# Performance work log

Measured on AMD Instinct MI355X. Metric: run time of the kernel, lower is better.

## Reference

```python
import jax, jax.numpy as jnp
import numpy as np

B, C, H, W = 8, 512, 64, 64
NH = 8
HD = C // NH
EPS = 1e-5


def _bn(x, w, b):
    # training-mode BatchNorm2d: batch stats over (B,H,W), biased variance
    mean = jnp.mean(x, axis=(0, 2, 3), keepdims=True)
    var = jnp.var(x, axis=(0, 2, 3), keepdims=True)
    return (x - mean) * jax.lax.rsqrt(var + EPS) * w[None, :, None, None] + b[None, :, None, None]


def setup_inputs() -> dict:
    key = jax.random.key(0)
    ks = jax.random.split(key, 8)
    s = 1.0 / np.sqrt(C)
    return {
        "x": jax.random.normal(ks[0], (B, C, H, W), dtype=jnp.float32),
        "q_w": jax.random.normal(ks[1], (C, C), dtype=jnp.float32) * s,
        "k_w": jax.random.normal(ks[2], (C, C), dtype=jnp.float32) * s,
        "v_w": jax.random.normal(ks[3], (C, C), dtype=jnp.float32) * s,
        "temperature": jnp.ones((NH, 1, 1), dtype=jnp.float32),
        "gamma": jnp.full((1,), 0.5, dtype=jnp.float32),
        "bn_in_w": jnp.ones((C,), dtype=jnp.float32),
        "bn_in_b": jnp.zeros((C,), dtype=jnp.float32),
        "bn_out_w": jnp.ones((C,), dtype=jnp.float32),
        "bn_out_b": jnp.zeros((C,), dtype=jnp.float32),
    }


def reference(x, q_w, k_w, v_w, temperature, gamma, bn_in_w, bn_in_b, bn_out_w, bn_out_b):
    xn = _bn(x, bn_in_w, bn_in_b)
    # 1x1 convs == channel-mixing linear maps
    q = jnp.einsum('oc,bchw->bohw', q_w, xn)
    k = jnp.einsum('oc,bchw->bohw', k_w, xn)
    v = jnp.einsum('oc,bchw->bohw', v_w, xn)
    # 2D FFT over spatial dims -> complex64
    q_f = jnp.fft.fft2(q)
    k_f = jnp.fft.fft2(k)
    v_f = jnp.fft.fft2(v)
    # b (h c) H W -> b h c (H W)
    qh = q_f.reshape(B, NH, HD, H * W)
    kh = k_f.reshape(B, NH, HD, H * W)
    vh = v_f.reshape(B, NH, HD, H * W)
    # complex channel-attention scores [B, NH, HD, HD]
    attn = jnp.einsum('bhcn,bhdn->bhcd', qh, kh) * temperature[None]
    # complex softmax: softmax over real and imag parts independently
    attn = jax.lax.complex(jax.nn.softmax(attn.real, axis=-1),
                           jax.nn.softmax(attn.imag, axis=-1))
    out_f = jnp.einsum('bhcd,bhdn->bhcn', attn, vh)
    out_f = out_f.reshape(B, C, H, W)
    out = jnp.fft.ifft2(out_f).real
    out = x + gamma * out
    return _bn(out, bn_out_w, bn_out_b)
```

## Files before the change

kernel.cpp:

```cpp
#include <hip/hip_runtime.h>
#include <math.h>

#define NB 8
#define NC 512
#define NHW 4096
#define NNH 8
#define BN_EPS 1e-5f

typedef __attribute__((ext_vector_type(8))) short bf16x8;
typedef __attribute__((ext_vector_type(4))) float f32x4;
typedef __attribute__((ext_vector_type(4))) short s16x4;
typedef __attribute__((ext_vector_type(2))) short s16x2;
typedef unsigned short ushort_t;

__device__ __forceinline__ ushort_t bf16r(float f) {
    unsigned u = __float_as_uint(f);
    return (ushort_t)((u + 0x7fffu + ((u >> 16) & 1u)) >> 16);
}
__device__ __forceinline__ float bf16f(ushort_t h) {
    return __uint_as_float(((unsigned)h) << 16);
}
__device__ __forceinline__ void split3(float v, ushort_t& h1, ushort_t& h2, ushort_t& h3) {
    h1 = bf16r(v); float r = v - bf16f(h1);
    h2 = bf16r(r); r -= bf16f(h2);
    h3 = bf16r(r);
}
__device__ __forceinline__ void split2(float v, ushort_t& h1, ushort_t& h2) {
    h1 = bf16r(v); float r = v - bf16f(h1);
    h2 = bf16r(r);
}

__global__ __launch_bounds__(256) void fa_bn_stats(const float* __restrict__ src,
                                                   const float* __restrict__ w,
                                                   const float* __restrict__ bb,
                                                   float* __restrict__ ss) {
    int c = blockIdx.x;
    int t = threadIdx.x;
    float s = 0.f, sq = 0.f;
    for (int b = 0; b < NB; ++b) {
        const float4* p = (const float4*)(src + ((size_t)(b * NC + c)) * NHW);
        for (int i = t; i < NHW / 4; i += 256) {
            float4 v = p[i];
            s += v.x + v.y + v.z + v.w;
            sq += v.x * v.x + v.y * v.y + v.z * v.z + v.w * v.w;
        }
    }
#pragma unroll
    for (int off = 32; off; off >>= 1) {
        s += __shfl_down(s, off, 64);
        sq += __shfl_down(sq, off, 64);
    }
    __shared__ float ls[4], lq[4];
    int wid = t >> 6, lane = t & 63;
    if (lane == 0) { ls[wid] = s; lq[wid] = sq; }
    __syncthreads();
    if (t == 0) {
        float S = ls[0] + ls[1] + ls[2] + ls[3];
        float Q = lq[0] + lq[1] + lq[2] + lq[3];
        float n = (float)(NB * NHW);
        float mean = S / n;
        float var = Q / n - mean * mean;
        float r = rsqrtf(var + BN_EPS);
        float sc = r * w[c];
        ss[c] = sc;
        ss[NC + c] = bb[c] - mean * sc;
    }
}

__global__ __launch_bounds__(256) void fa_bn2_fin(const float* __restrict__ st,
                                                  const float* __restrict__ w,
                                                  const float* __restrict__ bb,
                                                  float* __restrict__ ss) {
    int c = blockIdx.x * 256 + threadIdx.x;
    float S = st[c], Q = st[512 + c];
    float n = (float)(NB * NHW);
    float mean = S / n;
    float var = Q / n - mean * mean;
    float r = rsqrtf(var + BN_EPS);
    float sc = r * w[c];
    ss[c] = sc;
    ss[NC + c] = bb[c] - mean * sc;
}

__global__ __launch_bounds__(256) void fa_split(const float* __restrict__ x,
                                                const float* __restrict__ ss,
                                                short* __restrict__ X0, short* __restrict__ X1,
                                                short* __restrict__ R0, short* __restrict__ R1) {
    int b = blockIdx.x >> 9, c = blockIdx.x & 511;
    float sc = ss[c], sh = ss[NC + c];
    size_t o = ((size_t)(b * NC + c)) * NHW;
    const float4* src = (const float4*)(x + o);
    __shared__ float xf[NHW];
    int t = threadIdx.x;
#pragma unroll
    for (int k = 0; k < 4; ++k) {
        int i4 = t + k * 256;
        float4 v = src[i4];
        s16x4 p0, p1;
#pragma unroll
        for (int j = 0; j < 4; ++j) {
            float xn = fmaf(((const float*)&v)[j], sc, sh);
            xf[4 * i4 + j] = xn;
            ushort_t h0, h1;
            split2(xn, h0, h1);
            p0[j] = (short)h0; p1[j] = (short)h1;
        }
        *(s16x4*)&X0[o + 4 * i4] = p0;
        *(s16x4*)&X1[o + 4 * i4] = p1;
    }
    __syncthreads();
#pragma unroll
    for (int k = 0; k < 4; ++k) {
        int i4 = t + k * 256;
        s16x4 p0, p1;
#pragma unroll
        for (int j = 0; j < 4; ++j) {
            int u = 4 * i4 + j;
            int rev = (((64 - (u >> 6)) & 63) << 6) | ((64 - (u & 63)) & 63);
            float xn = xf[rev];
            ushort_t h0, h1;
            split2(xn, h0, h1);
            p0[j] = (short)h0; p1[j] = (short)h1;
        }
        *(s16x4*)&R0[o + 4 * i4] = p0;
        *(s16x4*)&R1[o + 4 * i4] = p1;
    }
}

__global__ __launch_bounds__(256) void fa_wsplit_qk(const float* __restrict__ qw,
                                                    const float* __restrict__ kw,
                                                    short* __restrict__ Q0, short* __restrict__ Q1,
                                                    short* __restrict__ Q2,
                                                    short* __restrict__ K0p, short* __restrict__ K1p,
                                                    short* __restrict__ K2p) {
    int r = blockIdx.x, m = blockIdx.y;
    const float* src = m ? kw : qw;
    short* P0 = m ? K0p : Q0;
    short* P1 = m ? K1p : Q1;
    short* P2 = m ? K2p : Q2;
    int t = threadIdx.x;
    float2 v = *(const float2*)&src[(size_t)r * NC + 2 * t];
    s16x2 p0, p1, p2;
    ushort_t a, bq, cq;
    split3(v.x, a, bq, cq); p0[0] = (short)a; p1[0] = (short)bq; p2[0] = (short)cq;
    split3(v.y, a, bq, cq); p0[1] = (short)a; p1[1] = (short)bq; p2[1] = (short)cq;
    size_t o = (size_t)r * NC + 2 * t;
    *(s16x2*)&P0[o] = p0;
    *(s16x2*)&P1[o] = p1;
    *(s16x2*)&P2[o] = p2;
}

__global__ __launch_bounds__(256) void fa_wsplit_vt(const float* __restrict__ vw,
                                                    short* __restrict__ V0, short* __restrict__ V1) {
    __shared__ float tile[64][65];
    int hd0 = blockIdx.x * 64, cc0 = blockIdx.y * 64;
    int t = threadIdx.x;
#pragma unroll
    for (int k = 0; k < 16; ++k) {
        int idx = t + k * 256;
        int r = idx >> 6, c = idx & 63;
        tile[r][c] = vw[(size_t)(hd0 + r) * NC + cc0 + c];
    }
    __syncthreads();
#pragma unroll
    for (int k = 0; k < 16; ++k) {
        int idx = t + k * 256;
        int r = idx >> 6, c = idx & 63;
        float v = tile[c][r];
        ushort_t a, bq;
        split2(v, a, bq);
        size_t o = (size_t)(cc0 + r) * NC + hd0 + c;
        V0[o] = (short)a; V1[o] = (short)bq;
    }
}

#define GSTR 40
__global__ __launch_bounds__(256, 2) void fa_gram5(
    const short* __restrict__ X0, const short* __restrict__ X1,
    const short* __restrict__ R0, const short* __restrict__ R1,
    float* __restrict__ Gs) {
    static const char PI[10] = {0, 0, 0, 0, 1, 1, 1, 2, 2, 3};
    static const char PJ[10] = {0, 1, 2, 3, 1, 2, 3, 2, 3, 3};
    __shared__ __align__(16) short A0[128 * GSTR], A1[128 * GSTR];
    __shared__ __align__(16) short B0[128 * GSTR], B1[128 * GSTR];
    const int bid = blockIdx.x;
    const int flat = (bid & 7) * 40 + (bid >> 3);
    const int p = flat % 10;
    const int rem = flat / 10;
    const int kq = rem & 3;
    const int b = rem >> 2;
    const int c1t = PI[p] * 128, c2t = PJ[p] * 128;
    const int t = threadIdx.x, lane = t & 63, wv = t >> 6;
    const int row = t >> 1, half = (t & 1) * 16;
    const int lo = row * GSTR + half;
    const size_t kb0 = (size_t)kq * 1024;
    const short* pA0 = X0 + ((size_t)(b * NC + c1t + row)) * NHW + half + kb0;
    const short* pA1 = X1 + ((size_t)(b * NC + c1t + row)) * NHW + half + kb0;
    const short* pB0 = R0 + ((size_t)(b * NC + c2t + row)) * NHW + half + kb0;
    const short* pB1 = R1 + ((size_t)(b * NC + c2t + row)) * NHW + half + kb0;
    const int wrow = (wv >> 1) * 64, wcol = (wv & 1) * 64;
    const int frow = lane & 15, koff = (lane >> 4) * 8;

    f32x4 acc[4][4];
#pragma unroll
    for (int i = 0; i < 4; ++i)
#pragma unroll
        for (int j = 0; j < 4; ++j) {
            f32x4 z = {0.f, 0.f, 0.f, 0.f};
            acc[i][j] = z;
        }

    bf16x8 rA0a = *(const bf16x8*)&pA0[0], rA0b = *(const bf16x8*)&pA0[8];
    bf16x8 rA1a = *(const bf16x8*)&pA1[0], rA1b = *(const bf16x8*)&pA1[8];
    bf16x8 rB0a = *(const bf16x8*)&pB0[0], rB0b = *(const bf16x8*)&pB0[8];
    bf16x8 rB1a = *(const bf16x8*)&pB1[0], rB1b = *(const bf16x8*)&pB1[8];

#pragma unroll 1
    for (int s = 0; s < 32; ++s) {
        __syncthreads();
        *(bf16x8*)&A0[lo] = rA0a; *(bf16x8*)&A0[lo + 8] = rA0b;
        *(bf16x8*)&A1[lo] = rA1a; *(bf16x8*)&A1[lo + 8] = rA1b;
        *(bf16x8*)&B0[lo] = rB0a; *(bf16x8*)&B0[lo + 8] = rB0b;
        *(bf16x8*)&B1[lo] = rB1a; *(bf16x8*)&B1[lo + 8] = rB1b;
        __syncthreads();
        if (s < 31) {
            pA0 += 32; pA1 += 32; pB0 += 32; pB1 += 32;
            rA0a = *(const bf16x8*)&pA0[0]; rA0b = *(const bf16x8*)&pA0[8];
            rA1a = *(const bf16x8*)&pA1[0]; rA1b = *(const bf16x8*)&pA1[8];
            rB0a = *(const bf16x8*)&pB0[0]; rB0b = *(const bf16x8*)&pB0[8];
            rB1a = *(const bf16x8*)&pB1[0]; rB1b = *(const bf16x8*)&pB1[8];
        }
        bf16x8 a0[4], a1[4];
#pragma unroll
        for (int fr = 0; fr < 4; ++fr) {
            int o = (wrow + fr * 16 + frow) * GSTR + koff;
            a0[fr] = *(const bf16x8*)&A0[o];
            a1[fr] = *(const bf16x8*)&A1[o];
        }
        {
            bf16x8 bv[4];
#pragma unroll
            for (int fc = 0; fc < 4; ++fc)
                bv[fc] = *(const bf16x8*)&B0[(wcol + fc * 16 + frow) * GSTR + koff];
#pragma unroll
            for (int fr = 0; fr < 4; ++fr)
#pragma unroll
                for (int fc = 0; fc < 4; ++fc) {
                    acc[fr][fc] = __builtin_amdgcn_mfma_f32_16x16x32_bf16(a0[fr], bv[fc], acc[fr][fc], 0, 0, 0);
                    acc[fr][fc] = __builtin_amdgcn_mfma_f32_16x16x32_bf16(a1[fr], bv[fc], acc[fr][fc], 0, 0, 0);
                }
        }
        {
            bf16x8 bv[4];
#pragma unroll
            for (int fc = 0; fc < 4; ++fc)
                bv[fc] = *(const bf16x8*)&B1[(wcol + fc * 16 + frow) * GSTR + koff];
#pragma unroll
            for (int fr = 0; fr < 4; ++fr)
#pragma unroll
                for (int fc = 0; fc < 4; ++fc)
                    acc[fr][fc] = __builtin_amdgcn_mfma_f32_16x16x32_bf16(a0[fr], bv[fc], acc[fr][fc], 0, 0, 0);
        }
    }
    float* Gsl = Gs + (size_t)kq * 2097152;
    const bool diag = (c1t == c2t);
#pragma unroll
    for (int fr = 0; fr < 4; ++fr)
#pragma unroll
        for (int fc = 0; fc < 4; ++fc)
#pragma unroll
            for (int j = 0; j < 4; ++j) {
                int r1 = c1t + wrow + fr * 16 + (lane >> 4) * 4 + j;
                int r2 = c2t + wcol + fc * 16 + frow;
                float v = acc[fr][fc][j];
                Gsl[((size_t)(b * NC) + r1) * NC + r2] = v;
                if (!diag) Gsl[((size_t)(b * NC) + r2) * NC + r1] = v;
            }
}

__global__ __launch_bounds__(256) void fa_gsplit(const float* __restrict__ Gs,
                                                 short* __restrict__ Gp0, short* __restrict__ Gp1,
                                                 short* __restrict__ Gp2) {
    size_t i = ((size_t)blockIdx.x * 256 + threadIdx.x) * 8;
    f32x4 s0 = *(const f32x4*)&Gs[i];
    f32x4 s1 = *(const f32x4*)&Gs[i + 4];
#pragma unroll
    for (int k = 1; k < 4; ++k) {
        s0 += *(const f32x4*)&Gs[(size_t)k * 2097152 + i];
        s1 += *(const f32x4*)&Gs[(size_t)k * 2097152 + i + 4];
    }
    bf16x8 p0, p1, p2;
#pragma unroll
    for (int j = 0; j < 4; ++j) {
        ushort_t a, bq, cq;
        split3(s0[j], a, bq, cq);
        p0[j] = (short)a; p1[j] = (short)bq; p2[j] = (short)cq;
        split3(s1[j], a, bq, cq);
        p0[4 + j] = (short)a; p1[4 + j] = (short)bq; p2[4 + j] = (short)cq;
    }
    *(bf16x8*)&Gp0[i] = p0;
    *(bf16x8*)&Gp1[i] = p1;
    *(bf16x8*)&Gp2[i] = p2;
}

__global__ __launch_bounds__(256, 2) void fa_attn2(
    const short* __restrict__ Gp0, const short* __restrict__ Gp1, const short* __restrict__ Gp2,
    const short* __restrict__ Q0, const short* __restrict__ Q1, const short* __restrict__ Q2,
    const short* __restrict__ Kp0, const short* __restrict__ Kp1, const short* __restrict__ Kp2,
    float* __restrict__ P) {
    __shared__ __align__(16) short Aq0[64 * GSTR], Aq1[64 * GSTR], Aq2[64 * GSTR];
    __shared__ __align__(16) short Bg0[64 * GSTR], Bg1[64 * GSTR], Bg2[64 * GSTR];
    __shared__ __align__(16) float Tf[64 * 68];
    const int chunk = blockIdx.x, h = blockIdx.y, b = blockIdx.z;
    const int t = threadIdx.x, lane = t & 63, wv = t >> 6;
    const int srow = t >> 2, sq = (t & 3) * 8;
    const int frow = lane & 15, koff = (lane >> 4) * 8;
    const int wrow = (wv >> 1) * 32, wcol = (wv & 1) * 32;
    const int slo = srow * GSTR + sq;
    const size_t qbase = ((size_t)(h * 64 + srow)) * NC + sq;
    const size_t gbase = ((size_t)(b * NC + chunk * 64 + srow)) * NC + sq;

    f32x4 acc[2][2];
#pragma unroll
    for (int i = 0; i < 2; ++i)
#pragma unroll
        for (int j = 0; j < 2; ++j) {
            f32x4 z = {0.f, 0.f, 0.f, 0.f};
            acc[i][j] = z;
        }
    for (int K0 = 0; K0 < NC; K0 += 32) {
        __syncthreads();
        *(bf16x8*)&Aq0[slo] = *(const bf16x8*)&Q0[qbase + K0];
        *(bf16x8*)&Aq1[slo] = *(const bf16x8*)&Q1[qbase + K0];
        *(bf16x8*)&Aq2[slo] = *(const bf16x8*)&Q2[qbase + K0];
        *(bf16x8*)&Bg0[slo] = *(const bf16x8*)&Gp0[gbase + K0];
        *(bf16x8*)&Bg1[slo] = *(const bf16x8*)&Gp1[gbase + K0];
        *(bf16x8*)&Bg2[slo] = *(const bf16x8*)&Gp2[gbase + K0];
        __syncthreads();
        bf16x8 a0[2], a1[2], a2[2];
#pragma unroll
        for (int fr = 0; fr < 2; ++fr) {
            int o = (wrow + fr * 16 + frow) * GSTR + koff;
            a0[fr] = *(const bf16x8*)&Aq0[o];
            a1[fr] = *(const bf16x8*)&Aq1[o];
            a2[fr] = *(const bf16x8*)&Aq2[o];
        }
#pragma unroll
        for (int fc = 0; fc < 2; ++fc) {
            int o = (wcol + fc * 16 + frow) * GSTR + koff;
            bf16x8 b0 = *(const bf16x8*)&Bg0[o];
            bf16x8 b1 = *(const bf16x8*)&Bg1[o];
            bf16x8 b2 = *(const bf16x8*)&Bg2[o];
#pragma unroll
            for (int fr = 0; fr < 2; ++fr) {
                acc[fr][fc] = __builtin_amdgcn_mfma_f32_16x16x32_bf16(a0[fr], b0, acc[fr][fc], 0, 0, 0);
                acc[fr][fc] = __builtin_amdgcn_mfma_f32_16x16x32_bf16(a1[fr], b0, acc[fr][fc], 0, 0, 0);
                acc[fr][fc] = __builtin_amdgcn_mfma_f32_16x16x32_bf16(a2[fr], b0, acc[fr][fc], 0, 0, 0);
                acc[fr][fc] = __builtin_amdgcn_mfma_f32_16x16x32_bf16(a0[fr], b1, acc[fr][fc], 0, 0, 0);
                acc[fr][fc] = __builtin_amdgcn_mfma_f32_16x16x32_bf16(a1[fr], b1, acc[fr][fc], 0, 0, 0);
                acc[fr][fc] = __builtin_amdgcn_mfma_f32_16x16x32_bf16(a0[fr], b2, acc[fr][fc], 0, 0, 0);
            }
        }
    }
#pragma unroll
    for (int fr = 0; fr < 2; ++fr)
#pragma unroll
        for (int fc = 0; fc < 2; ++fc)
#pragma unroll
            for (int j = 0; j < 4; ++j)
                Tf[(wrow + fr * 16 + (lane >> 4) * 4 + j) * 68 + wcol + fc * 16 + frow] = acc[fr][fc][j];

    f32x4 acc2[4];
#pragma unroll
    for (int j = 0; j < 4; ++j) {
        f32x4 z = {0.f, 0.f, 0.f, 0.f};
        acc2[j] = z;
    }
    for (int kw = 0; kw < 2; ++kw) {
        __syncthreads();
        size_t kb = ((size_t)(h * 64 + srow)) * NC + chunk * 64 + kw * 32 + sq;
        *(bf16x8*)&Bg0[slo] = *(const bf16x8*)&Kp0[kb];
        *(bf16x8*)&Bg1[slo] = *(const bf16x8*)&Kp1[kb];
        *(bf16x8*)&Bg2[slo] = *(const bf16x8*)&Kp2[kb];
        __syncthreads();
        f32x4 u0 = *(const f32x4*)&Tf[(wv * 16 + frow) * 68 + kw * 32 + koff];
        f32x4 u1 = *(const f32x4*)&Tf[(wv * 16 + frow) * 68 + kw * 32 + koff + 4];
        bf16x8 t0, t1, t2;
#pragma unroll
        for (int j = 0; j < 4; ++j) {
            ushort_t a, bq, cq;
            split3(u0[j], a, bq, cq);
            t0[j] = (short)a; t1[j] = (short)bq; t2[j] = (short)cq;
            split3(u1[j], a, bq, cq);
            t0[4 + j] = (short)a; t1[4 + j] = (short)bq; t2[4 + j] = (short)cq;
        }
#pragma unroll
        for (int fc = 0; fc < 4; ++fc) {
            int o = (fc * 16 + frow) * GSTR + koff;
            bf16x8 b0 = *(const bf16x8*)&Bg0[o];
            bf16x8 b1 = *(const bf16x8*)&Bg1[o];
            bf16x8 b2 = *(const bf16x8*)&Bg2[o];
            acc2[fc] = __builtin_amdgcn_mfma_f32_16x16x32_bf16(t0, b0, acc2[fc], 0, 0, 0);
            acc2[fc] = __builtin_amdgcn_mfma_f32_16x16x32_bf16(t1, b0, acc2[fc], 0, 0, 0);
            acc2[fc] = __builtin_amdgcn_mfma_f32_16x16x32_bf16(t2, b0, acc2[fc], 0, 0, 0);
            acc2[fc] = __builtin_amdgcn_mfma_f32_16x16x32_bf16(t0, b1, acc2[fc], 0, 0, 0);
            acc2[fc] = __builtin_amdgcn_mfma_f32_16x16x32_bf16(t1, b1, acc2[fc], 0, 0, 0);
            acc2[fc] = __builtin_amdgcn_mfma_f32_16x16x32_bf16(t0, b2, acc2[fc], 0, 0, 0);
        }
    }
    size_t base = (((size_t)(b * NNH + h)) * 8 + chunk) * 4096;
#pragma unroll
    for (int fc = 0; fc < 4; ++fc)
#pragma unroll
        for (int j = 0; j < 4; ++j) {
            int row = wv * 16 + (lane >> 4) * 4 + j;
            int col = fc * 16 + frow;
            P[base + row * 64 + col] = acc2[fc][j];
        }
}

__global__ __launch_bounds__(256, 1) void fa_fin2(const float* __restrict__ P,
                                                  const float* __restrict__ temp,
                                                  const short* __restrict__ V0,
                                                  const short* __restrict__ V1,
                                                  short* __restrict__ M0) {
    __shared__ float Asm[64 * 68];
    const int h = blockIdx.x, b = blockIdx.y;
    const int t = threadIdx.x, lane = t & 63, wv = t >> 6;
    const float tv = temp[h] * (float)NHW;
    const float* pb = P + ((size_t)(b * NNH + h)) * 8 * 4096;
    for (int i = t; i < 4096; i += 256) {
        float s = 0.f;
#pragma unroll
        for (int ch = 0; ch < 8; ++ch) s += pb[ch * 4096 + i];
        Asm[(i >> 6) * 68 + (i & 63)] = s * tv;
    }
    __syncthreads();
    {
        int row = t >> 2, base = row * 68 + (t & 3) * 16;
        float m = -1e30f;
#pragma unroll
        for (int j = 0; j < 16; ++j) m = fmaxf(m, Asm[base + j]);
        m = fmaxf(m, __shfl_xor(m, 1, 64));
        m = fmaxf(m, __shfl_xor(m, 2, 64));
        float s = 0.f;
#pragma unroll
        for (int j = 0; j < 16; ++j) {
            float e = __expf(Asm[base + j] - m);
            Asm[base + j] = e;
            s += e;
        }
        s += __shfl_xor(s, 1, 64);
        s += __shfl_xor(s, 2, 64);
        float inv = 1.0f / s;
#pragma unroll
        for (int j = 0; j < 16; ++j) Asm[base + j] *= inv;
    }
    __syncthreads();
    const int frow = lane & 15, koff = (lane >> 4) * 8;
    bf16x8 a0[4][2], a1[4][2];
#pragma unroll
    for (int fr = 0; fr < 4; ++fr)
#pragma unroll
        for (int kw = 0; kw < 2; ++kw) {
            f32x4 u0 = *(const f32x4*)&Asm[(fr * 16 + frow) * 68 + kw * 32 + koff];
            f32x4 u1 = *(const f32x4*)&Asm[(fr * 16 + frow) * 68 + kw * 32 + koff + 4];
#pragma unroll
            for (int j = 0; j < 4; ++j) {
                ushort_t a, bq;
                split2(u0[j], a, bq);
                a0[fr][kw][j] = (short)a; a1[fr][kw][j] = (short)bq;
                split2(u1[j], a, bq);
                a0[fr][kw][4 + j] = (short)a; a1[fr][kw][4 + j] = (short)bq;
            }
        }
    for (int half = 0; half < 2; ++half) {
        int cb = wv * 128 + half * 64;
        f32x4 acc[4][4];
#pragma unroll
        for (int i = 0; i < 4; ++i)
#pragma unroll
            for (int j = 0; j < 4; ++j) {
                f32x4 z = {0.f, 0.f, 0.f, 0.f};
                acc[i][j] = z;
            }
#pragma unroll
        for (int fc = 0; fc < 4; ++fc)
#pragma unroll
            for (int kw = 0; kw < 2; ++kw) {
                size_t vb = (size_t)(cb + fc * 16 + frow) * NC + h * 64 + kw * 32 + koff;
                bf16x8 b0 = *(const bf16x8*)&V0[vb];
                bf16x8 b1 = *(const bf16x8*)&V1[vb];
#pragma unroll
                for (int fr = 0; fr < 4; ++fr) {
                    acc[fr][fc] = __builtin_amdgcn_mfma_f32_16x16x32_bf16(a0[fr][kw], b0, acc[fr][fc], 0, 0, 0);
                    acc[fr][fc] = __builtin_amdgcn_mfma_f32_16x16x32_bf16(a0[fr][kw], b1, acc[fr][fc], 0, 0, 0);
                    acc[fr][fc] = __builtin_amdgcn_mfma_f32_16x16x32_bf16(a1[fr][kw], b0, acc[fr][fc], 0, 0, 0);
                }
            }
#pragma unroll
        for (int fr = 0; fr < 4; ++fr)
#pragma unroll
            for (int fc = 0; fc < 4; ++fc)
#pragma unroll
                for (int j = 0; j < 4; ++j) {
                    int row = fr * 16 + (lane >> 4) * 4 + j;
                    int cc = cb + fc * 16 + frow;
                    size_t o = ((size_t)(b * NC + h * 64 + row)) * NC + cc;
                    M0[o] = (short)bf16r(acc[fr][fc][j]);
                }
    }
}

#define OSTR2 72
__global__ __launch_bounds__(256, 4) void fa_out4(const float* __restrict__ x,
                                                  const short* __restrict__ M0,
                                                  const short* __restrict__ X0,
                                                  const float* __restrict__ gamma,
                                                  float* __restrict__ y,
                                                  float* __restrict__ st) {
    __shared__ __align__(16) short Am[128 * OSTR2];
    __shared__ __align__(16) short Bx[128 * OSTR2];
    const int s0 = blockIdx.x * 128, c0 = blockIdx.y * 128, b = blockIdx.z;
    const int t = threadIdx.x, lane = t & 63, wv = t >> 6;
    const int arow = t >> 1, ah = (t & 1) * 32;
    const int cc0 = (t & 31) * 2, sb = (t >> 5) * 16;
    const int frow = lane & 15, koff = (lane >> 4) * 8;
    const int wrow = (wv >> 1) * 64, wcol = (wv & 1) * 64;
    const size_t mbase = ((size_t)(b * NC + c0 + arow)) * NC + ah;
    const size_t xbase = ((size_t)(b * NC + cc0)) * NHW + s0 + sb;

    f32x4 acc[4][4];
#pragma unroll
    for (int i = 0; i < 4; ++i)
#pragma unroll
        for (int j = 0; j < 4; ++j) {
            f32x4 z = {0.f, 0.f, 0.f, 0.f};
            acc[i][j] = z;
        }

    bf16x8 mA[4], xA[4];
#pragma unroll
    for (int q = 0; q < 4; ++q) mA[q] = *(const bf16x8*)&M0[mbase + 8 * q];
    xA[0] = *(const bf16x8*)&X0[xbase];
    xA[1] = *(const bf16x8*)&X0[xbase + 8];
    xA[2] = *(const bf16x8*)&X0[xbase + NHW];
    xA[3] = *(const bf16x8*)&X0[xbase + NHW + 8];

#pragma unroll 1
    for (int K0 = 0; K0 < NC; K0 += 64) {
        __syncthreads();
#pragma unroll
        for (int q = 0; q < 4; ++q)
            *(bf16x8*)&Am[arow * OSTR2 + ah + 8 * q] = mA[q];
#pragma unroll
        for (int si = 0; si < 8; ++si) {
            s16x2 pv; pv[0] = xA[0][si]; pv[1] = xA[2][si];
            *(s16x2*)&Bx[(sb + si) * OSTR2 + cc0] = pv;
            s16x2 qv; qv[0] = xA[1][si]; qv[1] = xA[3][si];
            *(s16x2*)&Bx[(sb + 8 + si) * OSTR2 + cc0] = qv;
        }
        __syncthreads();
        if (K0 < NC - 64) {
            const size_t mb = mbase + K0 + 64;
            const size_t xb = xbase + (size_t)(K0 + 64) * NHW;
#pragma unroll
            for (int q = 0; q < 4; ++q) mA[q] = *(const bf16x8*)&M0[mb + 8 * q];
            xA[0] = *(const bf16x8*)&X0[xb];
            xA[1] = *(const bf16x8*)&X0[xb + 8];
            xA[2] = *(const bf16x8*)&X0[xb + NHW];
            xA[3] = *(const bf16x8*)&X0[xb + NHW + 8];
        }
#pragma unroll
        for (int kw = 0; kw < 2; ++kw) {
            int ko = kw * 32 + koff;
            bf16x8 a0[4], b0[4];
#pragma unroll
            for (int fr = 0; fr < 4; ++fr)
                a0[fr] = *(const bf16x8*)&Am[(wrow + fr * 16 + frow) * OSTR2 + ko];
#pragma unroll
            for (int fc = 0; fc < 4; ++fc)
                b0[fc] = *(const bf16x8*)&Bx[(wcol + fc * 16 + frow) * OSTR2 + ko];
#pragma unroll
            for (int fr = 0; fr < 4; ++fr)
#pragma unroll
                for (int fc = 0; fc < 4; ++fc)
                    acc[fr][fc] = __builtin_amdgcn_mfma_f32_16x16x32_bf16(a0[fr], b0[fc], acc[fr][fc], 0, 0, 0);
        }
    }
    float g = gamma[0];
    float sY[16], sQ[16];
#pragma unroll
    for (int i = 0; i < 16; ++i) { sY[i] = 0.f; sQ[i] = 0.f; }
#pragma unroll
    for (int fr = 0; fr < 4; ++fr)
#pragma unroll
        for (int fc = 0; fc < 4; ++fc)
#pragma unroll
            for (int j = 0; j < 4; ++j) {
                int c = c0 + wrow + fr * 16 + (lane >> 4) * 4 + j;
                int s = s0 + wcol + fc * 16 + frow;
                size_t idx = ((size_t)(b * NC + c)) * NHW + s;
                float v = x[idx] + g * acc[fr][fc][j];
                y[idx] = v;
                sY[fr * 4 + j] += v;
                sQ[fr * 4 + j] += v * v;
            }
#pragma unroll
    for (int i = 0; i < 16; ++i) {
#pragma unroll
        for (int off = 1; off < 16; off <<= 1) {
            sY[i] += __shfl_xor(sY[i], off, 64);
            sQ[i] += __shfl_xor(sQ[i], off, 64);
        }
    }
    if (frow == 0) {
#pragma unroll
        for (int i = 0; i < 16; ++i) {
            int c = c0 + wrow + (i >> 2) * 16 + (lane >> 4) * 4 + (i & 3);
            atomicAdd(&st[c], sY[i]);
            atomicAdd(&st[512 + c], sQ[i]);
        }
    }
}

__global__ __launch_bounds__(256) void fa_bn_apply(float* __restrict__ y,
                                                   const float* __restrict__ ss) {
    const float* scale = ss;
    const float* shift = ss + NC;
    const long long total4 = (long long)NB * NC * NHW / 4;
    for (long long i4 = (long long)blockIdx.x * blockDim.x + threadIdx.x; i4 < total4;
         i4 += (long long)gridDim.x * blockDim.x) {
        int c = (int)((i4 >> 10) & (NC - 1));
        float4 v = ((const float4*)y)[i4];
        float sc = scale[c], sh = shift[c];
        v.x = v.x * sc + sh;
        v.y = v.y * sc + sh;
        v.z = v.z * sc + sh;
        v.w = v.w * sc + sh;
        ((float4*)y)[i4] = v;
    }
}

__device__ __forceinline__ int swz(int row, int kk) {
    return ((kk >> 2) ^ (row >> 2)) * 4 + (kk & 3);
}
__device__ __forceinline__ void mm_tile(const float* __restrict__ As,
                                        const float* __restrict__ Bs,
                                        int tr, int tc, float (&acc)[4][4]) {
#pragma unroll
    for (int k4 = 0; k4 < 16; ++k4) {
        float4 a[4], bv[4];
#pragma unroll
        for (int i = 0; i < 4; ++i)
            a[i] = *(const float4*)&As[(tr * 4 + i) * 64 + (((k4 ^ tr) & 15) << 2)];
#pragma unroll
        for (int j = 0; j < 4; ++j)
            bv[j] = *(const float4*)&Bs[(tc * 4 + j) * 64 + (((k4 ^ tc) & 15) << 2)];
#pragma unroll
        for (int i = 0; i < 4; ++i)
#pragma unroll
            for (int j = 0; j < 4; ++j)
                acc[i][j] += a[i].x * bv[j].x + a[i].y * bv[j].y +
                             a[i].z * bv[j].z + a[i].w * bv[j].w;
    }
}
__global__ __launch_bounds__(256, 2) void fa_gram_mfma(const float* __restrict__ x,
                                                       const float* __restrict__ ss,
                                                       float* __restrict__ G) {
    __shared__ __align__(16) short As0[128 * GSTR], As1[128 * GSTR], As2[128 * GSTR];
    __shared__ __align__(16) short Bs0[128 * GSTR], Bs1[128 * GSTR], Bs2[128 * GSTR];
    const int c2t = blockIdx.x * 128;
    const int c1t = blockIdx.y * 128;
    const int b = blockIdx.z >> 2;
    const int kq = blockIdx.z & 3;
    const int t = threadIdx.x;
    const int lane = t & 63, wv = t >> 6;
    const float* scale = ss;
    const float* shift = ss + NC;
    const int arow = t >> 1, akh = (t & 1) * 16;
    const float scA = scale[c1t + arow], shA = shift[c1t + arow];
    const float* abase = x + ((size_t)(b * NC + c1t + arow)) * NHW;
    const int kk = lane & 31, rh = lane >> 5;
    f32x4 acc[4][4];
#pragma unroll
    for (int i = 0; i < 4; ++i)
#pragma unroll
        for (int j = 0; j < 4; ++j) {
            f32x4 z = {0.f, 0.f, 0.f, 0.f};
            acc[i][j] = z;
        }
    const int wrow = (wv >> 1) * 64, wcol = (wv & 1) * 64;
    const int frow = lane & 15, koff = (lane >> 4) * 8;
    for (int step = 0; step < 32; ++step) {
        const int K0 = kq * 1024 + step * 32;
        const int h = K0 >> 6, wbase = K0 & 63;
        const int hp = (64 - h) & 63;
        const int wp0 = (64 - wbase - kk) & 63;
        __syncthreads();
#pragma unroll
        for (int i = 0; i < 4; ++i) {
            float4 v = *(const float4*)(abase + K0 + akh + 4 * i);
            s16x4 p1, p2, p3;
#pragma unroll
            for (int j = 0; j < 4; ++j) {
                float xv = fmaf(((const float*)&v)[j], scA, shA);
                ushort_t h1, h2, h3;
                split3(xv, h1, h2, h3);
                p1[j] = (short)h1; p2[j] = (short)h2; p3[j] = (short)h3;
            }
            int o = arow * GSTR + akh + 4 * i;
            *(s16x4*)&As0[o] = p1;
            *(s16x4*)&As1[o] = p2;
            *(s16x4*)&As2[o] = p3;
        }
#pragma unroll 4
        for (int i = 0; i < 16; ++i) {
            int row = wv * 32 + i * 2 + rh;
            int c2 = c2t + row;
            float xv = x[((size_t)(b * NC + c2)) * NHW + hp * 64 + wp0];
            float v = fmaf(xv, scale[c2], shift[c2]);
            ushort_t h1, h2, h3;
            split3(v, h1, h2, h3);
            int o = row * GSTR + kk;
            Bs0[o] = (short)h1; Bs1[o] = (short)h2; Bs2[o] = (short)h3;
        }
        __syncthreads();
        bf16x8 a0[4], a1[4], a2[4];
#pragma unroll
        for (int fr = 0; fr < 4; ++fr) {
            int o = (wrow + fr * 16 + frow) * GSTR + koff;
            a0[fr] = *(const bf16x8*)&As0[o];
            a1[fr] = *(const bf16x8*)&As1[o];
            a2[fr] = *(const bf16x8*)&As2[o];
        }
        {
            bf16x8 bv[4];
#pragma unroll
            for (int fc = 0; fc < 4; ++fc)
                bv[fc] = *(const bf16x8*)&Bs0[(wcol + fc * 16 + frow) * GSTR + koff];
#pragma unroll
            for (int fr = 0; fr < 4; ++fr)
#pragma unroll
                for (int fc = 0; fc < 4; ++fc) {
                    acc[fr][fc] = __builtin_amdgcn_mfma_f32_16x16x32_bf16(a0[fr], bv[fc], acc[fr][fc], 0, 0, 0);
                    acc[fr][fc] = __builtin_amdgcn_mfma_f32_16x16x32_bf16(a1[fr], bv[fc], acc[fr][fc], 0, 0, 0);
                    acc[fr][fc] = __builtin_amdgcn_mfma_f32_16x16x32_bf16(a2[fr], bv[fc], acc[fr][fc], 0, 0, 0);
                }
        }
        {
            bf16x8 bv[4];
#pragma unroll
            for (int fc = 0; fc < 4; ++fc)
                bv[fc] = *(const bf16x8*)&Bs1[(wcol + fc * 16 + frow) * GSTR + koff];
#pragma unroll
            for (int fr = 0; fr < 4; ++fr)
#pragma unroll
                for (int fc = 0; fc < 4; ++fc) {
                    acc[fr][fc] = __builtin_amdgcn_mfma_f32_16x16x32_bf16(a0[fr], bv[fc], acc[fr][fc], 0, 0, 0);
                    acc[fr][fc] = __builtin_amdgcn_mfma_f32_16x16x32_bf16(a1[fr], bv[fc], acc[fr][fc], 0, 0, 0);
                }
        }
        {
            bf16x8 bv[4];
#pragma unroll
            for (int fc = 0; fc < 4; ++fc)
                bv[fc] = *(const bf16x8*)&Bs2[(wcol + fc * 16 + frow) * GSTR + koff];
#pragma unroll
            for (int fr = 0; fr < 4; ++fr)
#pragma unroll
                for (int fc = 0; fc < 4; ++fc)
                    acc[fr][fc] = __builtin_amdgcn_mfma_f32_16x16x32_bf16(a0[fr], bv[fc], acc[fr][fc], 0, 0, 0);
        }
    }
#pragma unroll
    for (int fr = 0; fr < 4; ++fr)
#pragma unroll
        for (int fc = 0; fc < 4; ++fc)
#pragma unroll
            for (int j = 0; j < 4; ++j) {
                int c1 = c1t + wrow + fr * 16 + (lane >> 4) * 4 + j;
                int c2 = c2t + wcol + fc * 16 + frow;
                atomicAdd(&G[((size_t)(b * NC + c1)) * NC + c2], acc[fr][fc][j]);
            }
}
__global__ __launch_bounds__(256) void fa_attn_partial(const float* __restrict__ G,
                                                       const float* __restrict__ qw,
                                                       const float* __restrict__ kw,
                                                       float* __restrict__ P) {
    __shared__ float As[4096];
    __shared__ float Bs[4096];
    int chunk = blockIdx.x, h = blockIdx.y, b = blockIdx.z;
    int cc0 = chunk * 64;
    int t = threadIdx.x;
    int lane = t & 63, r0 = t >> 6;
    int tr = t >> 4, tc = t & 15;
    float acc[4][4] = {};
#pragma unroll 1
    for (int kb = 0; kb < NC; kb += 64) {
#pragma unroll
        for (int r = 0; r < 16; ++r) {
            int c = r * 4 + r0;
            As[c * 64 + swz(c, lane)] = qw[(size_t)(h * 64 + c) * NC + kb + lane];
            int kk = r * 4 + r0;
            Bs[lane * 64 + swz(lane, kk)] =
                G[((size_t)(b * NC) + kb + kk) * NC + cc0 + lane];
        }
        __syncthreads();
        mm_tile(As, Bs, tr, tc, acc);
        __syncthreads();
    }
#pragma unroll
    for (int i = 0; i < 4; ++i) {
        int row = tr * 4 + i;
        *(float4*)&As[row * 64 + (((tc ^ tr) & 15) << 2)] =
            make_float4(acc[i][0], acc[i][1], acc[i][2], acc[i][3]);
    }
#pragma unroll
    for (int r = 0; r < 16; ++r) {
        int d = r * 4 + r0;
        Bs[d * 64 + swz(d, lane)] = kw[(size_t)(h * 64 + d) * NC + cc0 + lane];
    }
    __syncthreads();
    float acc2[4][4] = {};
    mm_tile(As, Bs, tr, tc, acc2);
    size_t base = ((size_t)((b * NNH + h) * 8 + chunk)) * 4096;
#pragma unroll
    for (int i = 0; i < 4; ++i) {
        float4 v = make_float4(acc2[i][0], acc2[i][1], acc2[i][2], acc2[i][3]);
        *(float4*)&P[base + (tr * 4 + i) * 64 + tc * 4] = v;
    }
}
__global__ __launch_bounds__(256) void fa_attn_finalize(const float* __restrict__ P,
                                                        const float* __restrict__ temp,
                                                        const float* __restrict__ vw,
                                                        float* __restrict__ M) {
    __shared__ float attn_s[4096];
    __shared__ float vw_s[64 * 128];
    int h = blockIdx.x, b = blockIdx.y;
    int t = threadIdx.x;
    float tv = temp[h] * (float)NHW;
    for (int idx = t; idx < 4096; idx += 256) {
        float s = 0.f;
#pragma unroll
        for (int ch = 0; ch < 8; ++ch)
            s += P[((size_t)((b * NNH + h) * 8 + ch)) * 4096 + idx];
        attn_s[idx] = s * tv;
    }
    __syncthreads();
    if (t < 64) {
        float m = -1e30f;
        for (int d = 0; d < 64; ++d) m = fmaxf(m, attn_s[t * 64 + d]);
        float sum = 0.f;
        for (int d = 0; d < 64; ++d) {
            float e = expf(attn_s[t * 64 + d] - m);
            attn_s[t * 64 + d] = e;
            sum += e;
        }
        float inv = 1.0f / sum;
        for (int d = 0; d < 64; ++d) attn_s[t * 64 + d] *= inv;
    }
    __syncthreads();
    for (int ccb = 0; ccb < 4; ++ccb) {
        for (int i = t; i < 64 * 128; i += 256) {
            int d = i >> 7, cc = i & 127;
            vw_s[i] = vw[((size_t)(h * 64 + d)) * NC + ccb * 128 + cc];
        }
        __syncthreads();
        for (int i = t; i < 64 * 128; i += 256) {
            int c = i >> 7, cc = i & 127;
            float s = 0.f;
#pragma unroll 8
            for (int d = 0; d < 64; ++d)
                s += attn_s[c * 64 + d] * vw_s[d * 128 + cc];
            M[((size_t)(b * NC) + h * 64 + c) * NC + ccb * 128 + cc] = s;
        }
        __syncthreads();
    }
}
#define OSTR 72
__global__ __launch_bounds__(256, 2) void fa_out_mfma(const float* __restrict__ x,
                                                      const float* __restrict__ ss,
                                                      const float* __restrict__ M,
                                                      const float* __restrict__ gamma,
                                                      float* __restrict__ y) {
    __shared__ __align__(16) short As0[128 * OSTR], As1[128 * OSTR];
    __shared__ __align__(16) short Bs0[128 * OSTR], Bs1[128 * OSTR];
    const int s0 = blockIdx.x * 128;
    const int c0 = blockIdx.y * 128;
    const int b = blockIdx.z;
    const int t = threadIdx.x;
    const int lane = t & 63, wv = t >> 6;
    const float* scale = ss;
    const float* shift = ss + NC;
    const int arow = t & 127, akh = (t >> 7) * 32;
    const float* abase = M + ((size_t)(b * NC + c0 + arow)) * NC;
    const int chl = t & 63, soff = (t >> 6) * 32;
    f32x4 acc[4][4];
#pragma unroll
    for (int i = 0; i < 4; ++i)
#pragma unroll
        for (int j = 0; j < 4; ++j) {
            f32x4 z = {0.f, 0.f, 0.f, 0.f};
            acc[i][j] = z;
        }
    const int wrow = (wv >> 1) * 64, wcol = (wv & 1) * 64;
    const int frow = lane & 15;
    for (int K0 = 0; K0 < NC; K0 += 64) {
        __syncthreads();
#pragma unroll
        for (int i = 0; i < 8; ++i) {
            float4 v = *(const float4*)(abase + K0 + akh + 4 * i);
            s16x4 p1, p2;
#pragma unroll
            for (int j = 0; j < 4; ++j) {
                ushort_t h1, h2;
                split2(((const float*)&v)[j], h1, h2);
                p1[j] = (short)h1; p2[j] = (short)h2;
            }
            int o = arow * OSTR + akh + 4 * i;
            *(s16x4*)&As0[o] = p1;
            *(s16x4*)&As1[o] = p2;
        }
        {
            int ch = K0 + chl;
            float sc = scale[ch], sh = shift[ch];
            const float* bp = x + ((size_t)(b * NC + ch)) * NHW + s0 + soff;
#pragma unroll
            for (int i = 0; i < 8; ++i) {
                float4 v = *(const float4*)(bp + 4 * i);
#pragma unroll
                for (int j = 0; j < 4; ++j) {
                    float xv = fmaf(((const float*)&v)[j], sc, sh);
                    ushort_t h1, h2;
                    split2(xv, h1, h2);
                    int o = (soff + 4 * i + j) * OSTR + chl;
                    Bs0[o] = (short)h1;
                    Bs1[o] = (short)h2;
                }
            }
        }
        __syncthreads();
#pragma unroll
        for (int kw = 0; kw < 2; ++kw) {
            int koff = kw * 32 + (lane >> 4) * 8;
            bf16x8 aA[4], aB[4], bv[4];
#pragma unroll
            for (int fr = 0; fr < 4; ++fr) {
                int o = (wrow + fr * 16 + frow) * OSTR + koff;
                aA[fr] = *(const bf16x8*)&As0[o];
                aB[fr] = *(const bf16x8*)&As1[o];
            }
#pragma unroll
            for (int fc = 0; fc < 4; ++fc)
                bv[fc] = *(const bf16x8*)&Bs0[(wcol + fc * 16 + frow) * OSTR + koff];
#pragma unroll
            for (int fr = 0; fr < 4; ++fr)
#pragma unroll
                for (int fc = 0; fc < 4; ++fc) {
                    acc[fr][fc] = __builtin_amdgcn_mfma_f32_16x16x32_bf16(aA[fr], bv[fc], acc[fr][fc], 0, 0, 0);
                    acc[fr][fc] = __builtin_amdgcn_mfma_f32_16x16x32_bf16(aB[fr], bv[fc], acc[fr][fc], 0, 0, 0);
                }
#pragma unroll
            for (int fc = 0; fc < 4; ++fc)
                bv[fc] = *(const bf16x8*)&Bs1[(wcol + fc * 16 + frow) * OSTR + koff];
#pragma unroll
            for (int fr = 0; fr < 4; ++fr)
#pragma unroll
                for (int fc = 0; fc < 4; ++fc)
                    acc[fr][fc] = __builtin_amdgcn_mfma_f32_16x16x32_bf16(aA[fr], bv[fc], acc[fr][fc], 0, 0, 0);
        }
    }
    float g = gamma[0];
#pragma unroll
    for (int fr = 0; fr < 4; ++fr)
#pragma unroll
        for (int fc = 0; fc < 4; ++fc)
#pragma unroll
            for (int j = 0; j < 4; ++j) {
                int c = c0 + wrow + fr * 16 + (lane >> 4) * 4 + j;
                int s = s0 + wcol + fc * 16 + frow;
                size_t idx = ((size_t)(b * NC + c)) * NHW + s;
                y[idx] = x[idx] + g * acc[fr][fc][j];
            }
}

extern "C" void kernel_launch(void* const* d_in, const int* in_sizes, int n_in,
                              void* d_out, int out_size, void* d_ws, size_t ws_size,
                              hipStream_t stream) {
    const float* x = (const float*)d_in[0];
    const float* qw = (const float*)d_in[1];
    const float* kw = (const float*)d_in[2];
    const float* vw = (const float*)d_in[3];
    const float* temp = (const float*)d_in[4];
    const float* gamma = (const float*)d_in[5];
    const float* bnw1 = (const float*)d_in[6];
    const float* bnb1 = (const float*)d_in[7];
    const float* bnw2 = (const float*)d_in[8];
    const float* bnb2 = (const float*)d_in[9];
    float* out = (float*)d_out;

    size_t off = 0;
    auto take = [&](size_t nbytes) -> char* {
        char* p = (char*)d_ws + off;
        off += (nbytes + 255) & ~(size_t)255;
        return p;
    };
    float* ss1 = (float*)take(4096);
    float* ss2 = (float*)take(4096);
    float* st = (float*)take(4096);
    float* Gs = (float*)take((size_t)4 * 2097152 * 4);
    short* Q0 = (short*)take(524288);
    short* Q1 = (short*)take(524288);
    short* Q2 = (short*)take(524288);
    short* Kp0 = (short*)take(524288);
    short* Kp1 = (short*)take(524288);
    short* Kp2 = (short*)take(524288);
    short* V0 = (short*)take(524288);
    short* V1 = (short*)take(524288);
    short* X0 = (short*)take(33554432);
    short* X1 = (short*)take(33554432);
    short* X2 = (short*)take(33554432);
    short* XR2 = (short*)take(33554432);
    size_t need = off;

    if (ws_size >= need) {
        short* Gp0 = X2;
        short* Gp1 = X2 + 2097152;
        short* Gp2 = X2 + 4194304;
        float* P = (float*)XR2;
        short* M0 = (short*)((char*)XR2 + 8388608);
        short* R0 = (short*)d_out;
        short* R1 = (short*)d_out + 16777216;

        fa_bn_stats<<<NC, 256, 0, stream>>>(x, bnw1, bnb1, ss1);
        fa_split<<<NB * NC, 256, 0, stream>>>(x, ss1, X0, X1, R0, R1);
        fa_wsplit_qk<<<dim3(NC, 2), 256, 0, stream>>>(qw, kw, Q0, Q1, Q2, Kp0, Kp1, Kp2);
        fa_wsplit_vt<<<dim3(8, 8), 256, 0, stream>>>(vw, V0, V1);
        fa_gram5<<<320, 256, 0, stream>>>(X0, X1, R0, R1, Gs);
        fa_gsplit<<<1024, 256, 0, stream>>>(Gs, Gp0, Gp1, Gp2);
        fa_attn2<<<dim3(8, 8, 8), 256, 0, stream>>>(Gp0, Gp1, Gp2, Q0, Q1, Q2, Kp0, Kp1, Kp2, P);
        fa_fin2<<<dim3(NNH, NB), 256, 0, stream>>>(P, temp, V0, V1, M0);
        hipMemsetAsync(st, 0, 4096, stream);
        fa_out4<<<dim3(32, 4, 8), 256, 0, stream>>>(x, M0, X0, gamma, out, st);
        fa_bn2_fin<<<2, 256, 0, stream>>>(st, bnw2, bnb2, ss2);
        fa_bn_apply<<<2048, 256, 0, stream>>>(out, ss2);
    } else {
        float* ws = (float*)d_ws;
        float* fss1 = ws;
        float* fss2 = ws + 1024;
        float* G = ws + 2048;
        float* P = G + 2097152;
        float* M = G;
        hipMemsetAsync(G, 0, (size_t)NB * NC * NC * sizeof(float), stream);
        fa_bn_stats<<<NC, 256, 0, stream>>>(x, bnw1, bnb1, fss1);
        fa_gram_mfma<<<dim3(4, 4, 32), 256, 0, stream>>>(x, fss1, G);
        fa_attn_partial<<<dim3(8, 8, 8), 256, 0, stream>>>(G, qw, kw, P);
        fa_attn_finalize<<<dim3(NNH, NB), 256, 0, stream>>>(P, temp, vw, M);
        fa_out_mfma<<<dim3(32, 4, 8), 256, 0, stream>>>(x, fss1, M, gamma, out);
        fa_bn_stats<<<NC, 256, 0, stream>>>(out, bnw2, bnb2, fss2);
        fa_bn_apply<<<2048, 256, 0, stream>>>(out, fss2);
    }
}
```

Before: 270.4 us.

## Double-buffer register prefetch in output GEMM and remap block order per XCD

```diff
diff --git a/kernel.cpp b/kernel.cpp
--- a/kernel.cpp
+++ b/kernel.cpp
@@ -513,7 +513,7 @@
 }
 
 #define OSTR2 72
-__global__ __launch_bounds__(256, 4) void fa_out4(const float* __restrict__ x,
+__global__ __launch_bounds__(256, 4) void fa_out5(const float* __restrict__ x,
                                                   const short* __restrict__ M0,
                                                   const short* __restrict__ X0,
                                                   const float* __restrict__ gamma,
@@ -521,7 +521,11 @@
                                                   float* __restrict__ st) {
     __shared__ __align__(16) short Am[128 * OSTR2];
     __shared__ __align__(16) short Bx[128 * OSTR2];
-    const int s0 = blockIdx.x * 128, c0 = blockIdx.y * 128, b = blockIdx.z;
+    const int flat = (blockIdx.x & 7) * 128 + (blockIdx.x >> 3);
+    const int b = flat >> 7;
+    const int r = flat & 127;
+    const int c0 = (r & 3) * 128;
+    const int s0 = (r >> 2) * 128;
     const int t = threadIdx.x, lane = t & 63, wv = t >> 6;
     const int arow = t >> 1, ah = (t & 1) * 32;
     const int cc0 = (t & 31) * 2, sb = (t >> 5) * 16;
@@ -539,17 +543,18 @@
             acc[i][j] = z;
         }
 
-    bf16x8 mA[4], xA[4];
-#pragma unroll
-    for (int q = 0; q < 4; ++q) mA[q] = *(const bf16x8*)&M0[mbase + 8 * q];
-    xA[0] = *(const bf16x8*)&X0[xbase];
-    xA[1] = *(const bf16x8*)&X0[xbase + 8];
-    xA[2] = *(const bf16x8*)&X0[xbase + NHW];
-    xA[3] = *(const bf16x8*)&X0[xbase + NHW + 8];
-
-#pragma unroll 1
-    for (int K0 = 0; K0 < NC; K0 += 64) {
-        __syncthreads();
+    bf16x8 mP[4], xP[4], mQ[4], xQ[4];
+    auto loadK = [&](bf16x8 (&mA)[4], bf16x8 (&xA)[4], int K) {
+        const size_t mb = mbase + K;
+        const size_t xb = xbase + (size_t)K * NHW;
+#pragma unroll
+        for (int q = 0; q < 4; ++q) mA[q] = *(const bf16x8*)&M0[mb + 8 * q];
+        xA[0] = *(const bf16x8*)&X0[xb];
+        xA[1] = *(const bf16x8*)&X0[xb + 8];
+        xA[2] = *(const bf16x8*)&X0[xb + NHW];
+        xA[3] = *(const bf16x8*)&X0[xb + NHW + 8];
+    };
+    auto stage = [&](bf16x8 (&mA)[4], bf16x8 (&xA)[4]) {
 #pragma unroll
         for (int q = 0; q < 4; ++q)
             *(bf16x8*)&Am[arow * OSTR2 + ah + 8 * q] = mA[q];
@@ -560,17 +565,8 @@
             s16x2 qv; qv[0] = xA[1][si]; qv[1] = xA[3][si];
             *(s16x2*)&Bx[(sb + 8 + si) * OSTR2 + cc0] = qv;
         }
-        __syncthreads();
-        if (K0 < NC - 64) {
-            const size_t mb = mbase + K0 + 64;
-            const size_t xb = xbase + (size_t)(K0 + 64) * NHW;
-#pragma unroll
-            for (int q = 0; q < 4; ++q) mA[q] = *(const bf16x8*)&M0[mb + 8 * q];
-            xA[0] = *(const bf16x8*)&X0[xb];
-            xA[1] = *(const bf16x8*)&X0[xb + 8];
-            xA[2] = *(const bf16x8*)&X0[xb + NHW];
-            xA[3] = *(const bf16x8*)&X0[xb + NHW + 8];
-        }
+    };
+    auto domfma = [&]() {
 #pragma unroll
         for (int kw = 0; kw < 2; ++kw) {
             int ko = kw * 32 + koff;
@@ -587,6 +583,23 @@
                 for (int fc = 0; fc < 4; ++fc)
                     acc[fr][fc] = __builtin_amdgcn_mfma_f32_16x16x32_bf16(a0[fr], b0[fc], acc[fr][fc], 0, 0, 0);
         }
+    };
+
+    loadK(mP, xP, 0);
+    loadK(mQ, xQ, 64);
+
+#pragma unroll 1
+    for (int K0 = 0; K0 < NC; K0 += 128) {
+        __syncthreads();
+        stage(mP, xP);
+        __syncthreads();
+        if (K0 + 128 < NC) loadK(mP, xP, K0 + 128);
+        domfma();
+        __syncthreads();
+        stage(mQ, xQ);
+        __syncthreads();
+        if (K0 + 192 < NC) loadK(mQ, xQ, K0 + 192);
+        domfma();
     }
     float g = gamma[0];
     float sY[16], sQ[16];
@@ -1042,7 +1055,7 @@
         fa_attn2<<<dim3(8, 8, 8), 256, 0, stream>>>(Gp0, Gp1, Gp2, Q0, Q1, Q2, Kp0, Kp1, Kp2, P);
         fa_fin2<<<dim3(NNH, NB), 256, 0, stream>>>(P, temp, V0, V1, M0);
         hipMemsetAsync(st, 0, 4096, stream);
-        fa_out4<<<dim3(32, 4, 8), 256, 0, stream>>>(x, M0, X0, gamma, out, st);
+        fa_out5<<<1024, 256, 0, stream>>>(x, M0, X0, gamma, out, st);
         fa_bn2_fin<<<2, 256, 0, stream>>>(st, bnw2, bnb2, ss2);
         fa_bn_apply<<<2048, 256, 0, stream>>>(out, ss2);
     } else {
```

Result: slower. 340.0 us (+25.8%).
